# Kernel optimization log

Hardware: AMD Instinct MI355X
Metric: run time of the kernel (lower is better)

Reference implementation:

```python
import jax, jax.numpy as jnp
import numpy as np

N_NODES = 50000
N_EDGES = 800000
D_IN = 128
D_OUT = 128


def setup_inputs() -> dict:
    key = jax.random.key(0)
    k1, k2, k3, k4, k5 = jax.random.split(key, 5)
    x = jax.random.normal(k1, (N_NODES, D_IN), dtype=jnp.float32)
    edge_index = jax.random.randint(k2, (2, N_EDGES), 0, N_NODES, dtype=jnp.int64)
    # PyG SAGEConv params: lin_l (neighbors, with bias), lin_r (root, no bias)
    scale = 1.0 / np.sqrt(D_IN)
    W_l = jax.random.uniform(k3, (D_OUT, D_IN), dtype=jnp.float32, minval=-scale, maxval=scale)
    b_l = jax.random.uniform(k4, (D_OUT,), dtype=jnp.float32, minval=-scale, maxval=scale)
    W_r = jax.random.uniform(k5, (D_OUT, D_IN), dtype=jnp.float32, minval=-scale, maxval=scale)
    return {"x": x, "edge_index": edge_index, "W_l": W_l, "b_l": b_l, "W_r": W_r}


def reference(x, edge_index, W_l, b_l, W_r):
    src, dst = edge_index[0], edge_index[1]
    # mean aggregation of neighbor (source) features into destination nodes
    msg = x[src]  # [E, D_IN]
    agg_sum = jax.ops.segment_sum(msg, dst, num_segments=N_NODES)  # [N, D_IN]
    deg = jax.ops.segment_sum(jnp.ones((N_EDGES,), dtype=x.dtype), dst, num_segments=N_NODES)
    agg = agg_sum / jnp.maximum(deg, 1.0)[:, None]  # isolated nodes -> 0
    # out = lin_l(agg) + lin_r(x); ReLU from SAGE_NET wrapper (active=True)
    out = agg @ W_l.T + b_l + x @ W_r.T
    return jax.nn.relu(out)
```

## Files before the change

### kernel.cpp

```cpp
#include <hip/hip_runtime.h>
#include <hip/hip_bf16.h>

#define NNODES 50000
#define NEDGES 800000
#define DD 128
#define WPITCH 129
#define NPART 8
#define PSIZE 6250
#define CAP 64

typedef unsigned int u32;
typedef unsigned short u16;
typedef short bf16x8 __attribute__((ext_vector_type(8)));
typedef float f32x4 __attribute__((ext_vector_type(4)));

union U4B8 {
    uint4 u;
    bf16x8 b;
};

__device__ __forceinline__ u32 f2b(float f) {
    u32 u = __float_as_uint(f);
    u32 rounding = 0x7fffu + ((u >> 16) & 1u);
    return (u + rounding) >> 16;
}

__global__ __launch_bounds__(256) void setup_k(
    const float* __restrict__ x, const float* __restrict__ Wl,
    const float* __restrict__ Wr, u32* __restrict__ wb,
    u32* __restrict__ xb, u32* __restrict__ deg) {
    int b = blockIdx.x, tid = threadIdx.x;
    if (b < 64) {
        int idx = b * 256 + tid;
        int o = idx >> 7, c = idx & 127, k0 = 2 * c;
        const float* src = (k0 < DD) ? (Wl + o * DD + k0) : (Wr + o * DD + (k0 - DD));
        wb[idx] = f2b(src[0]) | (f2b(src[1]) << 16);
    } else if (b < 260) {
        int i = (b - 64) * 256 + tid;
        if (i < NNODES) deg[i] = 0u;
    } else {
        int i = (b - 260) * 256 + tid;
        float2 v = ((const float2*)x)[i];
        xb[i] = f2b(v.x) | (f2b(v.y) << 16);
    }
}

__global__ __launch_bounds__(256) void fill_bucket_k(
    const int* __restrict__ ei, u32* __restrict__ deg,
    u32* __restrict__ slots) {
    u32 part = blockIdx.x & (NPART - 1);
    u32 e = (blockIdx.x >> 3) * 256u + threadIdx.x;
    if (e >= NEDGES) return;
    int dst = ei[NEDGES + e];
    if ((u32)(dst - part * PSIZE) < (u32)PSIZE) {
        u32 pos = atomicAdd(deg + dst, 1u);
        if (pos < CAP) slots[(size_t)dst * CAP + pos] = (u32)ei[e];
    }
}

__global__ __launch_bounds__(256) void gather_bucket_k(
    const u32* __restrict__ xb, const u32* __restrict__ slots,
    const u32* __restrict__ deg, u32* __restrict__ aggb) {
    u32 gid = blockIdx.x * 256u + threadIdx.x;
    u32 node = gid >> 6;
    u32 lane = gid & 63u;
    if (node >= NNODES) return;
    u32 d = deg[node];
    u32 cnt = min(d, (u32)CAP);
    u32 sv = slots[(size_t)node * CAP + lane];
    float a0 = 0.f, a1 = 0.f;
    u32 j = 0;
    for (; j + 8 <= cnt; j += 8) {
        u32 s0 = __shfl(sv, (int)(j + 0), 64);
        u32 s1 = __shfl(sv, (int)(j + 1), 64);
        u32 s2 = __shfl(sv, (int)(j + 2), 64);
        u32 s3 = __shfl(sv, (int)(j + 3), 64);
        u32 s4 = __shfl(sv, (int)(j + 4), 64);
        u32 s5 = __shfl(sv, (int)(j + 5), 64);
        u32 s6 = __shfl(sv, (int)(j + 6), 64);
        u32 s7 = __shfl(sv, (int)(j + 7), 64);
        u32 v0 = xb[(size_t)s0 * 64 + lane];
        u32 v1 = xb[(size_t)s1 * 64 + lane];
        u32 v2 = xb[(size_t)s2 * 64 + lane];
        u32 v3 = xb[(size_t)s3 * 64 + lane];
        u32 v4 = xb[(size_t)s4 * 64 + lane];
        u32 v5 = xb[(size_t)s5 * 64 + lane];
        u32 v6 = xb[(size_t)s6 * 64 + lane];
        u32 v7 = xb[(size_t)s7 * 64 + lane];
        a0 += __uint_as_float(v0 << 16);
        a1 += __uint_as_float(v0 & 0xffff0000u);
        a0 += __uint_as_float(v1 << 16);
        a1 += __uint_as_float(v1 & 0xffff0000u);
        a0 += __uint_as_float(v2 << 16);
        a1 += __uint_as_float(v2 & 0xffff0000u);
        a0 += __uint_as_float(v3 << 16);
        a1 += __uint_as_float(v3 & 0xffff0000u);
        a0 += __uint_as_float(v4 << 16);
        a1 += __uint_as_float(v4 & 0xffff0000u);
        a0 += __uint_as_float(v5 << 16);
        a1 += __uint_as_float(v5 & 0xffff0000u);
        a0 += __uint_as_float(v6 << 16);
        a1 += __uint_as_float(v6 & 0xffff0000u);
        a0 += __uint_as_float(v7 << 16);
        a1 += __uint_as_float(v7 & 0xffff0000u);
    }
    for (; j < cnt; ++j) {
        u32 sj = __shfl(sv, (int)j, 64);
        u32 v = xb[(size_t)sj * 64 + lane];
        a0 += __uint_as_float(v << 16);
        a1 += __uint_as_float(v & 0xffff0000u);
    }
    float inv = 1.0f / fmaxf((float)d, 1.0f);
    aggb[(size_t)node * 64 + lane] = f2b(a0 * inv) | (f2b(a1 * inv) << 16);
}

__global__ __launch_bounds__(256) void mfma_fused_k(
    const u32* __restrict__ aggb, const u32* __restrict__ xb,
    const u32* __restrict__ wb, const float* __restrict__ bl,
    float* __restrict__ out) {
    __shared__ u32 w_lds[DD * WPITCH];
    __shared__ float sbias[DD];
    const int tid = threadIdx.x;
    for (int r = tid >> 5; r < DD; r += 8) {
        int c = (tid & 31) * 4;
        uint4 v = *(const uint4*)&wb[r * DD + c];
        *(uint4*)&w_lds[r * WPITCH + c] = v;
    }
    if (tid < DD) sbias[tid] = bl[tid];
    __syncthreads();

    const int wave = tid >> 6, lane = tid & 63;
    const int m = lane & 15, quad = lane >> 4;
    const int row0 = blockIdx.x * 128 + wave * 32;

    f32x4 acc[2][8];
#pragma unroll
    for (int t = 0; t < 2; ++t)
#pragma unroll
        for (int nt = 0; nt < 8; ++nt) acc[t][nt] = (f32x4){0.f, 0.f, 0.f, 0.f};

    for (int ks = 0; ks < 8; ++ks) {
        const u32* A = (ks < 4) ? aggb : xb;
        const int kc = (ks & 3) * 16 + quad * 4;
        U4B8 af[2];
#pragma unroll
        for (int t = 0; t < 2; ++t) {
            int r = row0 + t * 16 + m;
            r = r < NNODES ? r : NNODES - 1;
            af[t].u = *(const uint4*)&A[(size_t)r * 64 + kc];
        }
#pragma unroll
        for (int nt = 0; nt < 8; ++nt) {
            U4B8 bf;
            bf.u = *(const uint4*)&w_lds[(nt * 16 + m) * WPITCH + ks * 16 + quad * 4];
            acc[0][nt] = __builtin_amdgcn_mfma_f32_16x16x32_bf16(
                af[0].b, bf.b, acc[0][nt], 0, 0, 0);
            acc[1][nt] = __builtin_amdgcn_mfma_f32_16x16x32_bf16(
                af[1].b, bf.b, acc[1][nt], 0, 0, 0);
        }
    }
#pragma unroll
    for (int t = 0; t < 2; ++t) {
#pragma unroll
        for (int nt = 0; nt < 8; ++nt) {
            int col = nt * 16 + m;
            float b = sbias[col];
#pragma unroll
            for (int r = 0; r < 4; ++r) {
                int row = row0 + t * 16 + quad * 4 + r;
                if (row < NNODES)
                    out[(size_t)row * DD + col] = fmaxf(acc[t][nt][r] + b, 0.f);
            }
        }
    }
}

__global__ __launch_bounds__(256) void scatter_k(
    const float* __restrict__ x, const int* __restrict__ ei,
    float* __restrict__ agg, u32* __restrict__ deg) {
    u32 gid = blockIdx.x * 256u + threadIdx.x;
    u32 edge = gid >> 6;
    u32 lane = gid & 63u;
    if (edge >= NEDGES) return;
    int src = ei[edge];
    int dst = ei[NEDGES + edge];
    float2 v = ((const float2*)(x + (size_t)src * DD))[lane];
    float* p = agg + (size_t)dst * DD + lane * 2u;
    unsafeAtomicAdd(p, v.x);
    unsafeAtomicAdd(p + 1, v.y);
    if (lane == 0) atomicAdd(deg + dst, 1u);
}

__global__ __launch_bounds__(256) void mean_k(
    float* __restrict__ agg, const u32* __restrict__ deg) {
    u32 gid = blockIdx.x * 256u + threadIdx.x;
    u32 node = gid >> 6;
    u32 lane = gid & 63u;
    if (node >= NNODES) return;
    float inv = 1.0f / fmaxf((float)deg[node], 1.0f);
    float2* p = (float2*)(agg + (size_t)node * DD) + lane;
    float2 v = *p;
    *p = make_float2(v.x * inv, v.y * inv);
}

__global__ __launch_bounds__(256) void lin_l_k(
    float* __restrict__ agg,
    const float* __restrict__ Wl, const float* __restrict__ bl) {
    __shared__ u32 WT[DD * 65];
    __shared__ float rows[4 * DD];
    __shared__ float sbias[DD];
    const int tid = threadIdx.x;
    {
        u16* WTs = (u16*)WT;
        for (int i = tid; i < DD * DD; i += 256) {
            int o = i >> 7, k = i & 127;
            WTs[k * 130 + o] = (u16)f2b(Wl[i]);
        }
        if (tid < DD) sbias[tid] = bl[tid];
    }
    __syncthreads();
    const int h = tid & 63;
    const int nl = tid >> 6;
    for (int base = blockIdx.x * 4; base < NNODES; base += gridDim.x * 4) {
        ((float2*)rows)[tid] =
            ((const float2*)(agg + (size_t)(base + (tid >> 6)) * DD))[tid & 63];
        __syncthreads();
        float acc0 = sbias[2 * h], acc1 = sbias[2 * h + 1];
#pragma unroll
        for (int k = 0; k < DD; ++k) {
            float a = rows[nl * DD + k];
            u32 w2 = WT[k * 65 + h];
            acc0 = fmaf(a, __uint_as_float(w2 << 16), acc0);
            acc1 = fmaf(a, __uint_as_float(w2 & 0xffff0000u), acc1);
        }
        __syncthreads();
        ((float2*)(agg + (size_t)(base + nl) * DD))[h] = make_float2(acc0, acc1);
    }
}

__global__ __launch_bounds__(256) void lin_r_k(
    float* __restrict__ io, const float* __restrict__ x,
    const float* __restrict__ Wr) {
    __shared__ u32 WT[DD * 65];
    __shared__ float rows[4 * DD];
    const int tid = threadIdx.x;
    {
        u16* WTs = (u16*)WT;
        for (int i = tid; i < DD * DD; i += 256) {
            int o = i >> 7, k = i & 127;
            WTs[k * 130 + o] = (u16)f2b(Wr[i]);
        }
    }
    __syncthreads();
    const int h = tid & 63;
    const int nl = tid >> 6;
    for (int base = blockIdx.x * 4; base < NNODES; base += gridDim.x * 4) {
        ((float2*)rows)[tid] =
            ((const float2*)(x + (size_t)(base + (tid >> 6)) * DD))[tid & 63];
        __syncthreads();
        float2 t2 = ((const float2*)(io + (size_t)(base + nl) * DD))[h];
        float acc0 = t2.x, acc1 = t2.y;
#pragma unroll
        for (int k = 0; k < DD; ++k) {
            float a = rows[nl * DD + k];
            u32 w2 = WT[k * 65 + h];
            acc0 = fmaf(a, __uint_as_float(w2 << 16), acc0);
            acc1 = fmaf(a, __uint_as_float(w2 & 0xffff0000u), acc1);
        }
        acc0 = fmaxf(acc0, 0.f);
        acc1 = fmaxf(acc1, 0.f);
        __syncthreads();
        ((float2*)(io + (size_t)(base + nl) * DD))[h] = make_float2(acc0, acc1);
    }
}

extern "C" void kernel_launch(void* const* d_in, const int* in_sizes, int n_in,
                              void* d_out, int out_size, void* d_ws, size_t ws_size,
                              hipStream_t stream) {
    const float* x  = (const float*)d_in[0];
    const int*   ei = (const int*)d_in[1];
    const float* Wl = (const float*)d_in[2];
    const float* bl = (const float*)d_in[3];
    const float* Wr = (const float*)d_in[4];

    u32* deg   = (u32*)d_ws;
    u32* slots = deg + NNODES;
    u32* wb    = slots + (size_t)NNODES * CAP;
    u32* xb    = wb + 16384;
    u32* aggb  = xb + (size_t)NNODES * 64;
    const size_t need =
        ((size_t)NNODES * (1 + CAP + 64 + 64) + 16384) * 4;

    if (ws_size >= need) {
        setup_k<<<12760, 256, 0, stream>>>(x, Wl, Wr, wb, xb, deg);
        fill_bucket_k<<<3125 * NPART, 256, 0, stream>>>(ei, deg, slots);
        gather_bucket_k<<<12500, 256, 0, stream>>>(xb, slots, deg, aggb);
        mfma_fused_k<<<(NNODES + 127) / 128, 256, 0, stream>>>(
            aggb, xb, wb, bl, (float*)d_out);
    } else {
        float* agg = (float*)d_out;
        hipMemsetAsync(d_out, 0, (size_t)NNODES * DD * sizeof(float), stream);
        hipMemsetAsync(d_ws, 0, (size_t)NNODES * sizeof(u32), stream);
        scatter_k<<<(NEDGES * 64) / 256, 256, 0, stream>>>(x, ei, agg, deg);
        mean_k<<<(NNODES * 64 + 255) / 256, 256, 0, stream>>>(agg, deg);
        lin_l_k<<<1024, 256, 0, stream>>>(agg, Wl, bl);
        lin_r_k<<<1024, 256, 0, stream>>>(agg, x, Wr);
    }
}
```

Measured before the change: 174.4 us.

## Fuse bucket fill with bf16 conversion and gather two neighbors per wave

The separate setup and bucket-fill kernels become one kernel whose block ranges do edge bucketing, x-to-bf16 conversion and weight packing. The degree array is now zeroed with a memset. The gather kernel now has each half-wave load a different neighbor row with 8-byte loads, so two neighbors are fetched per instruction. The two halves are combined with a cross-lane shuffle at the end. This cuts one kernel launch and the number of load instructions in the gather, at the cost of a memset call and an extra shuffle reduction.

```diff
diff --git a/kernel.cpp b/kernel.cpp
--- a/kernel.cpp
+++ b/kernel.cpp
@@ -8,6 +8,9 @@
 #define NPART 8
 #define PSIZE 6250
 #define CAP 64
+#define FILL_B 25000
+#define XCV_B 12500
+#define WB_B 64
 
 typedef unsigned int u32;
 typedef unsigned short u16;
@@ -24,41 +27,38 @@
     u32 rounding = 0x7fffu + ((u >> 16) & 1u);
     return (u + rounding) >> 16;
 }
-
-__global__ __launch_bounds__(256) void setup_k(
-    const float* __restrict__ x, const float* __restrict__ Wl,
-    const float* __restrict__ Wr, u32* __restrict__ wb,
-    u32* __restrict__ xb, u32* __restrict__ deg) {
-    int b = blockIdx.x, tid = threadIdx.x;
-    if (b < 64) {
-        int idx = b * 256 + tid;
+__device__ __forceinline__ float blo(u32 v) { return __uint_as_float(v << 16); }
+__device__ __forceinline__ float bhi(u32 v) {
+    return __uint_as_float(v & 0xffff0000u);
+}
+
+__global__ __launch_bounds__(256) void work_k(
+    const int* __restrict__ ei, u32* __restrict__ deg, u32* __restrict__ slots,
+    const float* __restrict__ x, u32* __restrict__ xb,
+    const float* __restrict__ Wl, const float* __restrict__ Wr,
+    u32* __restrict__ wb) {
+    const int b = blockIdx.x, tid = threadIdx.x;
+    if (b < FILL_B) {
+        u32 part = (u32)b & (NPART - 1);
+        u32 e = ((u32)b >> 3) * 256u + tid;
+        int dst = ei[NEDGES + e];
+        if ((u32)(dst - part * PSIZE) < (u32)PSIZE) {
+            u32 pos = atomicAdd(deg + dst, 1u);
+            if (pos < CAP) slots[(size_t)dst * CAP + pos] = (u32)ei[e];
+        }
+    } else if (b < FILL_B + XCV_B) {
+        int i = (b - FILL_B) * 256 + tid;
+        float2 v = ((const float2*)x)[i];
+        xb[i] = f2b(v.x) | (f2b(v.y) << 16);
+    } else {
+        int idx = (b - FILL_B - XCV_B) * 256 + tid;
         int o = idx >> 7, c = idx & 127, k0 = 2 * c;
         const float* src = (k0 < DD) ? (Wl + o * DD + k0) : (Wr + o * DD + (k0 - DD));
         wb[idx] = f2b(src[0]) | (f2b(src[1]) << 16);
-    } else if (b < 260) {
-        int i = (b - 64) * 256 + tid;
-        if (i < NNODES) deg[i] = 0u;
-    } else {
-        int i = (b - 260) * 256 + tid;
-        float2 v = ((const float2*)x)[i];
-        xb[i] = f2b(v.x) | (f2b(v.y) << 16);
-    }
-}
-
-__global__ __launch_bounds__(256) void fill_bucket_k(
-    const int* __restrict__ ei, u32* __restrict__ deg,
-    u32* __restrict__ slots) {
-    u32 part = blockIdx.x & (NPART - 1);
-    u32 e = (blockIdx.x >> 3) * 256u + threadIdx.x;
-    if (e >= NEDGES) return;
-    int dst = ei[NEDGES + e];
-    if ((u32)(dst - part * PSIZE) < (u32)PSIZE) {
-        u32 pos = atomicAdd(deg + dst, 1u);
-        if (pos < CAP) slots[(size_t)dst * CAP + pos] = (u32)ei[e];
-    }
-}
-
-__global__ __launch_bounds__(256) void gather_bucket_k(
+    }
+}
+
+__global__ __launch_bounds__(256) void gather_pair_k(
     const u32* __restrict__ xb, const u32* __restrict__ slots,
     const u32* __restrict__ deg, u32* __restrict__ aggb) {
     u32 gid = blockIdx.x * 256u + threadIdx.x;
@@ -68,50 +68,58 @@
     u32 d = deg[node];
     u32 cnt = min(d, (u32)CAP);
     u32 sv = slots[(size_t)node * CAP + lane];
-    float a0 = 0.f, a1 = 0.f;
+    const u32 half = lane >> 5;
+    const u32 q = lane & 31u;
+    float a0 = 0.f, a1 = 0.f, a2 = 0.f, a3 = 0.f;
     u32 j = 0;
-    for (; j + 8 <= cnt; j += 8) {
-        u32 s0 = __shfl(sv, (int)(j + 0), 64);
-        u32 s1 = __shfl(sv, (int)(j + 1), 64);
-        u32 s2 = __shfl(sv, (int)(j + 2), 64);
-        u32 s3 = __shfl(sv, (int)(j + 3), 64);
-        u32 s4 = __shfl(sv, (int)(j + 4), 64);
-        u32 s5 = __shfl(sv, (int)(j + 5), 64);
-        u32 s6 = __shfl(sv, (int)(j + 6), 64);
-        u32 s7 = __shfl(sv, (int)(j + 7), 64);
-        u32 v0 = xb[(size_t)s0 * 64 + lane];
-        u32 v1 = xb[(size_t)s1 * 64 + lane];
-        u32 v2 = xb[(size_t)s2 * 64 + lane];
-        u32 v3 = xb[(size_t)s3 * 64 + lane];
-        u32 v4 = xb[(size_t)s4 * 64 + lane];
-        u32 v5 = xb[(size_t)s5 * 64 + lane];
-        u32 v6 = xb[(size_t)s6 * 64 + lane];
-        u32 v7 = xb[(size_t)s7 * 64 + lane];
-        a0 += __uint_as_float(v0 << 16);
-        a1 += __uint_as_float(v0 & 0xffff0000u);
-        a0 += __uint_as_float(v1 << 16);
-        a1 += __uint_as_float(v1 & 0xffff0000u);
-        a0 += __uint_as_float(v2 << 16);
-        a1 += __uint_as_float(v2 & 0xffff0000u);
-        a0 += __uint_as_float(v3 << 16);
-        a1 += __uint_as_float(v3 & 0xffff0000u);
-        a0 += __uint_as_float(v4 << 16);
-        a1 += __uint_as_float(v4 & 0xffff0000u);
-        a0 += __uint_as_float(v5 << 16);
-        a1 += __uint_as_float(v5 & 0xffff0000u);
-        a0 += __uint_as_float(v6 << 16);
-        a1 += __uint_as_float(v6 & 0xffff0000u);
-        a0 += __uint_as_float(v7 << 16);
-        a1 += __uint_as_float(v7 & 0xffff0000u);
-    }
-    for (; j < cnt; ++j) {
-        u32 sj = __shfl(sv, (int)j, 64);
-        u32 v = xb[(size_t)sj * 64 + lane];
-        a0 += __uint_as_float(v << 16);
-        a1 += __uint_as_float(v & 0xffff0000u);
-    }
-    float inv = 1.0f / fmaxf((float)d, 1.0f);
-    aggb[(size_t)node * 64 + lane] = f2b(a0 * inv) | (f2b(a1 * inv) << 16);
+    for (; j + 16 <= cnt; j += 16) {
+        uint2 v[8];
+#pragma unroll
+        for (int p = 0; p < 8; ++p) {
+            u32 sA = __shfl(sv, (int)(j + 2 * p), 64);
+            u32 sB = __shfl(sv, (int)(j + 2 * p + 1), 64);
+            u32 s = half ? sB : sA;
+            v[p] = *(const uint2*)&xb[(size_t)s * 64 + q * 2];
+        }
+#pragma unroll
+        for (int p = 0; p < 8; ++p) {
+            a0 += blo(v[p].x);
+            a1 += bhi(v[p].x);
+            a2 += blo(v[p].y);
+            a3 += bhi(v[p].y);
+        }
+    }
+    for (; j + 2 <= cnt; j += 2) {
+        u32 sA = __shfl(sv, (int)j, 64);
+        u32 sB = __shfl(sv, (int)(j + 1), 64);
+        u32 s = half ? sB : sA;
+        uint2 v = *(const uint2*)&xb[(size_t)s * 64 + q * 2];
+        a0 += blo(v.x);
+        a1 += bhi(v.x);
+        a2 += blo(v.y);
+        a3 += bhi(v.y);
+    }
+    if (j < cnt) {
+        u32 sA = __shfl(sv, (int)j, 64);
+        uint2 v = *(const uint2*)&xb[(size_t)sA * 64 + q * 2];
+        if (!half) {
+            a0 += blo(v.x);
+            a1 += bhi(v.x);
+            a2 += blo(v.y);
+            a3 += bhi(v.y);
+        }
+    }
+    a0 += __shfl_xor(a0, 32, 64);
+    a1 += __shfl_xor(a1, 32, 64);
+    a2 += __shfl_xor(a2, 32, 64);
+    a3 += __shfl_xor(a3, 32, 64);
+    if (lane < 32) {
+        float inv = 1.0f / fmaxf((float)d, 1.0f);
+        uint2 o;
+        o.x = f2b(a0 * inv) | (f2b(a1 * inv) << 16);
+        o.y = f2b(a2 * inv) | (f2b(a3 * inv) << 16);
+        *(uint2*)&aggb[(size_t)node * 64 + q * 2] = o;
+    }
 }
 
 __global__ __launch_bounds__(256) void mfma_fused_k(
@@ -292,9 +300,10 @@
         ((size_t)NNODES * (1 + CAP + 64 + 64) + 16384) * 4;
 
     if (ws_size >= need) {
-        setup_k<<<12760, 256, 0, stream>>>(x, Wl, Wr, wb, xb, deg);
-        fill_bucket_k<<<3125 * NPART, 256, 0, stream>>>(ei, deg, slots);
-        gather_bucket_k<<<12500, 256, 0, stream>>>(xb, slots, deg, aggb);
+        hipMemsetAsync(deg, 0, (size_t)NNODES * sizeof(u32), stream);
+        work_k<<<FILL_B + XCV_B + WB_B, 256, 0, stream>>>(
+            ei, deg, slots, x, xb, Wl, Wr, wb);
+        gather_pair_k<<<12500, 256, 0, stream>>>(xb, slots, deg, aggb);
         mfma_fused_k<<<(NNODES + 127) / 128, 256, 0, stream>>>(
             aggb, xb, wb, bl, (float*)d_out);
     } else {
```

Result: no change. 173.5 us (-0.5%).
